# Kernel optimization log

Hardware: AMD Instinct MI355X
Metric: run time of the kernel (lower is better)

## Reference

```python
import jax, jax.numpy as jnp
import numpy as np

B, S, E, HEAD = 8, 2048, 512, 64  # head_size = embeddings_dims // no_of_heads = 512 // 8


def setup_inputs() -> dict:
    key = jax.random.key(0)
    kx, kq, kk, kv, kl = jax.random.split(key, 5)
    x = jax.random.normal(kx, (B, S, E), dtype=jnp.float32)
    # Linear(512 -> 64, bias=False); store as [E, HEAD] so y = x @ W
    Wq = jax.random.normal(kq, (E, HEAD), dtype=jnp.float32) * (E ** -0.5)
    Wk = jax.random.normal(kk, (E, HEAD), dtype=jnp.float32) * (E ** -0.5)
    Wv = jax.random.normal(kv, (E, HEAD), dtype=jnp.float32) * (E ** -0.5)
    # Realistic padding mask: 1 for first `length` tokens, 0 after.
    lengths = jax.random.randint(kl, (B,), S // 2, S + 1)
    mask = (jnp.arange(S)[None, :] < lengths[:, None]).astype(jnp.int32)
    return {"x": x, "Wq": Wq, "Wk": Wk, "Wv": Wv, "mask": mask}


def reference(x, Wq, Wk, Wv, mask):
    # q, k, v: [B, S, HEAD]
    q = x @ Wq
    k = x @ Wk
    v = x @ Wv
    # scores: [B, S, S], scaled by head_size**-0.5 (k.shape[-1] in the original)
    scores = jnp.einsum('bqd,bkd->bqk', q, k) * (HEAD ** -0.5)
    causal = jnp.tril(jnp.ones((S, S), dtype=bool))            # [S, S]
    keep = (mask[:, None, :] != 0) & causal[None, :, :]        # padding mask broadcast over query rows, then causal
    scores = jnp.where(keep, scores, -jnp.inf)
    attn = jax.nn.softmax(scores, axis=-1)                     # [B, S, S]
    out = attn @ v                                             # [B, S, HEAD]
    return out
```

## Files before the change

kernel.cpp:

```cpp
#include <hip/hip_runtime.h>

#define BB 8
#define SS 2048
#define EE 512
#define HD 64
#define CHUNK 256
#define KT 64
#define NCH 8
#define PST 72
#define TST 72
#define XRS 40
#define XKB 1280
#define NITEMS 576

typedef __attribute__((ext_vector_type(8))) short bf16x8;
typedef __attribute__((ext_vector_type(4))) float f32x4;

static __device__ __forceinline__ unsigned short f2bf(float f) {
    unsigned u = __builtin_bit_cast(unsigned, f);
    u = (u + 0x7fffu + ((u >> 16) & 1u)) >> 16;
    return (unsigned short)u;
}
static __device__ __forceinline__ unsigned short f2bf_trunc(float f) {
    return (unsigned short)(__builtin_bit_cast(unsigned, f) >> 16);
}
static __device__ __forceinline__ float bf2f(unsigned short h) {
    unsigned u = ((unsigned)h) << 16;
    return __builtin_bit_cast(float, u);
}

__global__ __launch_bounds__(256) void pack_w_kernel(
    const float* __restrict__ Wq, const float* __restrict__ Wk, const float* __restrict__ Wv,
    unsigned short* __restrict__ Wt) {
    int tid = blockIdx.x * 256 + threadIdx.x;
    if (tid >= 3 * EE * HD) return;
    int w_idx = tid / (EE * HD);
    int rem = tid % (EE * HD);
    int kk = rem / HD, n = rem % HD;
    const float* Wsrc = (w_idx == 0) ? Wq : ((w_idx == 1) ? Wk : Wv);
    float val = Wsrc[kk * HD + n];
    if (w_idx == 0) val *= 0.125f;
    int kb = kk >> 5, kr = kk & 31, quad = kr >> 3, j = kr & 7;
    int t = n >> 4, c = n & 15;
    int lane = quad * 16 + c;
    Wt[w_idx * (EE * HD) + ((kb * 4 + t) * 64 + lane) * 8 + j] = f2bf(val);
}

__global__ __launch_bounds__(256) void qkv_kernel(
    const float* __restrict__ x,
    const unsigned short* __restrict__ Wt,
    unsigned short* __restrict__ q,
    unsigned short* __restrict__ k,
    unsigned short* __restrict__ vT) {
    __shared__ __align__(16) unsigned short Xs[16 * XKB];
    const int tid = threadIdx.x;
    const int lane = tid & 63;
    const int t = tid >> 6;
    const int c = lane & 15, quad = lane >> 4;
    const int r0 = blockIdx.x * 32;

    const float* xt = x + (size_t)r0 * EE;
#pragma unroll
    for (int i = 0; i < 16; ++i) {
        int fi = i * 256 + tid;
        int e4 = fi * 4;
        float4 v4 = *(const float4*)(xt + e4);
        int row = e4 >> 9, col = e4 & 511;
        int kb = col >> 5, cc = col & 31;
        ushort4 pk;
        pk.x = f2bf(v4.x); pk.y = f2bf(v4.y); pk.z = f2bf(v4.z); pk.w = f2bf(v4.w);
        *(ushort4*)(&Xs[kb * XKB + row * XRS + cc]) = pk;
    }
    __syncthreads();

    f32x4 acc[2][3];
#pragma unroll
    for (int rt = 0; rt < 2; ++rt)
        for (int m = 0; m < 3; ++m) acc[rt][m] = (f32x4){0.f, 0.f, 0.f, 0.f};

    const unsigned short* wbase0 = Wt + t * 512 + lane * 8;
#pragma unroll
    for (int kb = 0; kb < EE / 32; ++kb) {
        const unsigned short* wb = wbase0 + kb * 2048;
        bf16x8 bfrag[3];
#pragma unroll
        for (int m = 0; m < 3; ++m) bfrag[m] = *(const bf16x8*)(wb + m * (EE * HD));
#pragma unroll
        for (int rt = 0; rt < 2; ++rt) {
            bf16x8 afrag = *(const bf16x8*)(&Xs[kb * XKB + (rt * 16 + c) * XRS + quad * 8]);
#pragma unroll
            for (int m = 0; m < 3; ++m)
                acc[rt][m] = __builtin_amdgcn_mfma_f32_16x16x32_bf16(afrag, bfrag[m], acc[rt][m], 0, 0, 0);
        }
    }

    const int col = t * 16 + c;
#pragma unroll
    for (int rt = 0; rt < 2; ++rt) {
        const int rb = r0 + rt * 16;
        for (int r = 0; r < 4; ++r) {
            int row = rb + quad * 4 + r;
            q[(size_t)row * HD + col] = f2bf(acc[rt][0][r]);
            k[(size_t)row * HD + col] = f2bf(acc[rt][1][r]);
        }
        int row = rb + quad * 4;
        int b_ = row >> 11, sb = row & (SS - 1);
        ushort4 pk;
        pk.x = f2bf(acc[rt][2][0]); pk.y = f2bf(acc[rt][2][1]);
        pk.z = f2bf(acc[rt][2][2]); pk.w = f2bf(acc[rt][2][3]);
        *(ushort4*)(vT + ((size_t)b_ * HD + col) * SS + sb) = pk;
    }
}

__global__ __launch_bounds__(256, 3) void attn_kernel(
    const unsigned short* __restrict__ q,
    const unsigned short* __restrict__ k,
    const unsigned short* __restrict__ vT,
    const int* __restrict__ mask,
    unsigned short* __restrict__ po,
    float* __restrict__ pl,
    float* __restrict__ out) {
    __shared__ __align__(16) unsigned short Ks[2][64 * TST];
    __shared__ __align__(16) unsigned short Vs[2][64 * TST];
    __shared__ __align__(16) unsigned short Ps[4][16 * PST];
    const int tid = threadIdx.x;
    const int lane = tid & 63, wave = tid >> 6;
    const int c = lane & 15, quad = lane >> 4;

    int t = NITEMS - 1 - blockIdx.x;
    const int b_ = t / 72;
    int r = t % 72;
    int g = 0;
    while ((g + 1) * (g + 2) <= r) ++g;
    int rr = r - g * (g + 1);
    const int Q = 2 * g + rr / (g + 1);
    const int cx = rr % (g + 1);
    const int kstart = cx * CHUNK;
    const int kend = min(kstart + CHUNK, Q * 128 + 128);
    const int ntiles = (kend - kstart) >> 6;
    const int nch_active = Q / 2 + 1;
    const int r0 = Q * 128 + wave * 32;

    const unsigned short* qb_p = q + (size_t)b_ * SS * HD;
    const unsigned short* kb_p = k + (size_t)b_ * SS * HD;
    const unsigned short* vb = vT + (size_t)b_ * HD * SS;
    const int* mb = mask + b_ * SS;

    bf16x8 aq[2][2];
#pragma unroll
    for (int rt = 0; rt < 2; ++rt) {
        const unsigned short* qrow = qb_p + (size_t)(r0 + rt * 16 + c) * HD + quad * 8;
        aq[rt][0] = *(const bf16x8*)(qrow);
        aq[rt][1] = *(const bf16x8*)(qrow + 32);
    }

    f32x4 o[2][4];
    float l_i[2][4];
#pragma unroll
    for (int rt = 0; rt < 2; ++rt)
        for (int tt = 0; tt < 4; ++tt) {
            o[rt][tt] = (f32x4){0.f, 0.f, 0.f, 0.f};
            l_i[rt][tt] = 0.f;
        }

    bf16x8 sk[2], sv[2];
    auto stage_load = [&](int k0) {
        const unsigned short* ksrc = kb_p + (size_t)k0 * HD;
#pragma unroll
        for (int rnd = 0; rnd < 2; ++rnd) {
            int e = (rnd * 256 + tid) * 8;
            sk[rnd] = *(const bf16x8*)(ksrc + e);
            int t8 = rnd * 256 + tid;
            int vr = t8 >> 3, vc = (t8 & 7) * 8;
            sv[rnd] = *(const bf16x8*)(vb + (size_t)vr * SS + k0 + vc);
        }
    };
    auto stage_write = [&](int buf) {
        unsigned short* kd = &Ks[buf][0];
        unsigned short* vd = &Vs[buf][0];
#pragma unroll
        for (int rnd = 0; rnd < 2; ++rnd) {
            int e = (rnd * 256 + tid) * 8;
            int krow = e >> 6, kcol = e & 63;
            *(bf16x8*)(kd + krow * TST + kcol) = sk[rnd];
            int t8 = rnd * 256 + tid;
            int vr = t8 >> 3, vc = (t8 & 7) * 8;
            *(bf16x8*)(vd + vr * TST + vc) = sv[rnd];
        }
    };

    stage_load(kstart);
    stage_write(0);
    for (int kt = 0; kt < ntiles; ++kt) {
        __syncthreads();
        const int k0 = kstart + kt * KT;
        const bool pre = (kt + 1 < ntiles);
        if (pre) stage_load(k0 + KT);
        const unsigned short* ks = &Ks[kt & 1][0];
        const unsigned short* vs = &Vs[kt & 1][0];

        bool mk4[4];
#pragma unroll
        for (int kg = 0; kg < 4; ++kg) mk4[kg] = (mb[k0 + kg * 16 + c] != 0);

        bf16x8 kf[4][2];
#pragma unroll
        for (int kg = 0; kg < 4; ++kg) {
            kf[kg][0] = *(const bf16x8*)(ks + (kg * 16 + c) * TST + quad * 8);
            kf[kg][1] = *(const bf16x8*)(ks + (kg * 16 + c) * TST + 32 + quad * 8);
        }

        bf16x8 pa[2][2];
#pragma unroll
        for (int rt = 0; rt < 2; ++rt) {
            const int rbase = r0 + rt * 16;
            const bool fullc = (k0 + KT <= rbase);
            f32x4 accs4[4];
            __builtin_amdgcn_s_setprio(1);
#pragma unroll
            for (int kg = 0; kg < 4; ++kg) {
                f32x4 a = (f32x4){0.f, 0.f, 0.f, 0.f};
                a = __builtin_amdgcn_mfma_f32_16x16x32_bf16(aq[rt][0], kf[kg][0], a, 0, 0, 0);
                a = __builtin_amdgcn_mfma_f32_16x16x32_bf16(aq[rt][1], kf[kg][1], a, 0, 0, 0);
                accs4[kg] = a;
            }
            __builtin_amdgcn_s_setprio(0);
            unsigned short* pbuf = &Ps[wave][0];
#pragma unroll
            for (int kg = 0; kg < 4; ++kg) {
                int key = k0 + kg * 16 + c;
                bool mk = mk4[kg];
#pragma unroll
                for (int rr2 = 0; rr2 < 4; ++rr2) {
                    int row = rbase + quad * 4 + rr2;
                    bool keep = mk && (fullc || key <= row);
                    float e = __expf(fminf(accs4[kg][rr2], 80.f));
                    float pe = keep ? e : 0.f;
                    l_i[rt][rr2] += pe;
                    pbuf[(quad * 4 + rr2) * PST + kg * 16 + c] = f2bf_trunc(pe);
                }
            }
            pa[rt][0] = *(const bf16x8*)(pbuf + c * PST + quad * 8);
            pa[rt][1] = *(const bf16x8*)(pbuf + c * PST + 32 + quad * 8);
        }

#pragma unroll
        for (int tt = 0; tt < 4; ++tt) {
            bf16x8 bv0 = *(const bf16x8*)(vs + (tt * 16 + c) * TST + quad * 8);
            bf16x8 bv1 = *(const bf16x8*)(vs + (tt * 16 + c) * TST + 32 + quad * 8);
            __builtin_amdgcn_s_setprio(1);
#pragma unroll
            for (int rt = 0; rt < 2; ++rt) {
                o[rt][tt] = __builtin_amdgcn_mfma_f32_16x16x32_bf16(pa[rt][0], bv0, o[rt][tt], 0, 0, 0);
                o[rt][tt] = __builtin_amdgcn_mfma_f32_16x16x32_bf16(pa[rt][1], bv1, o[rt][tt], 0, 0, 0);
            }
            __builtin_amdgcn_s_setprio(0);
        }

        if (pre) stage_write((kt + 1) & 1);
    }

#pragma unroll
    for (int rt = 0; rt < 2; ++rt)
        for (int rr2 = 0; rr2 < 4; ++rr2) {
            float s = l_i[rt][rr2];
            s += __shfl_xor(s, 1);
            s += __shfl_xor(s, 2);
            s += __shfl_xor(s, 4);
            s += __shfl_xor(s, 8);
            l_i[rt][rr2] = s;
        }

    if (nch_active == 1) {
#pragma unroll
        for (int rt = 0; rt < 2; ++rt)
            for (int rr2 = 0; rr2 < 4; ++rr2) {
                int row = r0 + rt * 16 + quad * 4 + rr2;
                float l = l_i[rt][rr2];
                float inv = (l > 0.f) ? 1.f / l : 0.f;
                for (int tt = 0; tt < 4; ++tt)
                    out[((size_t)b_ * SS + row) * HD + tt * 16 + c] = o[rt][tt][rr2] * inv;
            }
        return;
    }

#pragma unroll
    for (int rt = 0; rt < 2; ++rt)
        for (int rr2 = 0; rr2 < 4; ++rr2) {
            int row_abs = r0 + rt * 16 + quad * 4 + rr2;
            int qb_i = row_abs >> 6, rl = row_abs & 63;
            size_t base = (size_t)(b_ * 32 + qb_i) * NCH + cx;
            float l = l_i[rt][rr2];
            float inv = (l > 0.f) ? 1.f / l : 0.f;
            for (int tt = 0; tt < 4; ++tt)
                po[base * 4096 + (size_t)rl * 64 + tt * 16 + c] = f2bf(o[rt][tt][rr2] * inv);
            if (c == 0) pl[base * 64 + rl] = l;
        }
}

__global__ __launch_bounds__(256) void combine_kernel(
    const unsigned short* __restrict__ po,
    const float* __restrict__ pl,
    float* __restrict__ out) {
    int t = blockIdx.x * 256 + threadIdx.x;
    if (t >= BB * (SS - 256) * (HD / 4)) return;
    int d4 = (t & 15) * 4;
    int rg = t >> 4;
    int b_ = rg / (SS - 256);
    int row = 256 + rg % (SS - 256);
    int qb = row >> 6, rl = row & 63;
    int nch = row / CHUNK + 1;
    size_t base = (size_t)(b_ * 32 + qb) * NCH;
    float L = 0.f;
    float acc0 = 0.f, acc1 = 0.f, acc2 = 0.f, acc3 = 0.f;
    for (int cc = 0; cc < nch; ++cc) {
        float l = pl[(base + cc) * 64 + rl];
        L += l;
        ushort4 pk = *(const ushort4*)(po + (base + cc) * 4096 + (size_t)rl * 64 + d4);
        acc0 += l * bf2f(pk.x);
        acc1 += l * bf2f(pk.y);
        acc2 += l * bf2f(pk.z);
        acc3 += l * bf2f(pk.w);
    }
    float inv = (L > 0.f) ? 1.f / L : 0.f;
    float4 o4;
    o4.x = acc0 * inv; o4.y = acc1 * inv; o4.z = acc2 * inv; o4.w = acc3 * inv;
    *(float4*)(out + ((size_t)b_ * SS + row) * HD + d4) = o4;
}

extern "C" void kernel_launch(void* const* d_in, const int* in_sizes, int n_in,
                              void* d_out, int out_size, void* d_ws, size_t ws_size,
                              hipStream_t stream) {
    const float* x = (const float*)d_in[0];
    const float* Wq = (const float*)d_in[1];
    const float* Wk = (const float*)d_in[2];
    const float* Wv = (const float*)d_in[3];
    const int* mask = (const int*)d_in[4];
    float* out = (float*)d_out;

    unsigned short* ws = (unsigned short*)d_ws;
    unsigned short* Wt = ws;
    unsigned short* q = Wt + 3 * EE * HD;
    unsigned short* kk = q + (size_t)BB * SS * HD;
    unsigned short* vT = kk + (size_t)BB * SS * HD;
    unsigned short* po = vT + (size_t)BB * SS * HD;
    float* pl = (float*)(po + (size_t)BB * 32 * NCH * 4096);

    pack_w_kernel<<<dim3((3 * EE * HD + 255) / 256), dim3(256), 0, stream>>>(Wq, Wk, Wv, Wt);
    qkv_kernel<<<dim3(BB * SS / 32), dim3(256), 0, stream>>>(x, Wt, q, kk, vT);
    attn_kernel<<<dim3(NITEMS), dim3(256), 0, stream>>>(q, kk, vT, mask, po, pl, out);
    combine_kernel<<<dim3((BB * (SS - 256) * (HD / 4) + 255) / 256), dim3(256), 0, stream>>>(po, pl, out);
}
```

Baseline: 109.1 us.

## Swap MFMA operand order to produce transposed tiles for vectorized stores

Swaps the A and B operands of the MFMA calls in the QKV projection and in both attention matmuls, so each lane holds four consecutive columns of one row instead of one column across four rows. This allows vectorized ushort4/float4 stores for q, k, output and partials, a packed uint2 write of P into shared memory, int4 mask loads, and a row-sum reduction of two shuffles instead of four per row. The vT store becomes four scalar strided stores, which may cost more in the projection kernel.

```diff
diff --git a/kernel.cpp b/kernel.cpp
--- a/kernel.cpp
+++ b/kernel.cpp
@@ -7,8 +7,8 @@
 #define CHUNK 256
 #define KT 64
 #define NCH 8
-#define PST 72
 #define TST 72
+#define PS32 36
 #define XRS 40
 #define XKB 1280
 #define NITEMS 576
@@ -21,12 +21,14 @@
     u = (u + 0x7fffu + ((u >> 16) & 1u)) >> 16;
     return (unsigned short)u;
 }
-static __device__ __forceinline__ unsigned short f2bf_trunc(float f) {
-    return (unsigned short)(__builtin_bit_cast(unsigned, f) >> 16);
-}
 static __device__ __forceinline__ float bf2f(unsigned short h) {
     unsigned u = ((unsigned)h) << 16;
     return __builtin_bit_cast(float, u);
+}
+static __device__ __forceinline__ unsigned pack2(float lo, float hi) {
+    unsigned ulo = __builtin_bit_cast(unsigned, lo) >> 16;
+    unsigned uhi = __builtin_bit_cast(unsigned, hi) & 0xffff0000u;
+    return uhi | ulo;
 }
 
 __global__ __launch_bounds__(256) void pack_w_kernel(
@@ -82,33 +84,33 @@
 #pragma unroll
     for (int kb = 0; kb < EE / 32; ++kb) {
         const unsigned short* wb = wbase0 + kb * 2048;
-        bf16x8 bfrag[3];
-#pragma unroll
-        for (int m = 0; m < 3; ++m) bfrag[m] = *(const bf16x8*)(wb + m * (EE * HD));
+        bf16x8 wfrag[3];
+#pragma unroll
+        for (int m = 0; m < 3; ++m) wfrag[m] = *(const bf16x8*)(wb + m * (EE * HD));
 #pragma unroll
         for (int rt = 0; rt < 2; ++rt) {
-            bf16x8 afrag = *(const bf16x8*)(&Xs[kb * XKB + (rt * 16 + c) * XRS + quad * 8]);
+            bf16x8 xfrag = *(const bf16x8*)(&Xs[kb * XKB + (rt * 16 + c) * XRS + quad * 8]);
 #pragma unroll
             for (int m = 0; m < 3; ++m)
-                acc[rt][m] = __builtin_amdgcn_mfma_f32_16x16x32_bf16(afrag, bfrag[m], acc[rt][m], 0, 0, 0);
-        }
-    }
-
-    const int col = t * 16 + c;
+                acc[rt][m] = __builtin_amdgcn_mfma_f32_16x16x32_bf16(wfrag[m], xfrag, acc[rt][m], 0, 0, 0);
+        }
+    }
+
+    const int colq = t * 16 + quad * 4;
 #pragma unroll
     for (int rt = 0; rt < 2; ++rt) {
-        const int rb = r0 + rt * 16;
-        for (int r = 0; r < 4; ++r) {
-            int row = rb + quad * 4 + r;
-            q[(size_t)row * HD + col] = f2bf(acc[rt][0][r]);
-            k[(size_t)row * HD + col] = f2bf(acc[rt][1][r]);
-        }
-        int row = rb + quad * 4;
+        const int row = r0 + rt * 16 + c;
+        ushort4 pq, pkk;
+        pq.x = f2bf(acc[rt][0][0]); pq.y = f2bf(acc[rt][0][1]);
+        pq.z = f2bf(acc[rt][0][2]); pq.w = f2bf(acc[rt][0][3]);
+        pkk.x = f2bf(acc[rt][1][0]); pkk.y = f2bf(acc[rt][1][1]);
+        pkk.z = f2bf(acc[rt][1][2]); pkk.w = f2bf(acc[rt][1][3]);
+        *(ushort4*)(q + (size_t)row * HD + colq) = pq;
+        *(ushort4*)(k + (size_t)row * HD + colq) = pkk;
         int b_ = row >> 11, sb = row & (SS - 1);
-        ushort4 pk;
-        pk.x = f2bf(acc[rt][2][0]); pk.y = f2bf(acc[rt][2][1]);
-        pk.z = f2bf(acc[rt][2][2]); pk.w = f2bf(acc[rt][2][3]);
-        *(ushort4*)(vT + ((size_t)b_ * HD + col) * SS + sb) = pk;
+#pragma unroll
+        for (int r = 0; r < 4; ++r)
+            vT[((size_t)b_ * HD + colq + r) * SS + sb] = f2bf(acc[rt][2][r]);
     }
 }
 
@@ -122,7 +124,7 @@
     float* __restrict__ out) {
     __shared__ __align__(16) unsigned short Ks[2][64 * TST];
     __shared__ __align__(16) unsigned short Vs[2][64 * TST];
-    __shared__ __align__(16) unsigned short Ps[4][16 * PST];
+    __shared__ __align__(16) unsigned int Ps32[4][16 * PS32];
     const int tid = threadIdx.x;
     const int lane = tid & 63, wave = tid >> 6;
     const int c = lane & 15, quad = lane >> 4;
@@ -155,13 +157,10 @@
     }
 
     f32x4 o[2][4];
-    float l_i[2][4];
+    float l_part[2] = {0.f, 0.f};
 #pragma unroll
     for (int rt = 0; rt < 2; ++rt)
-        for (int tt = 0; tt < 4; ++tt) {
-            o[rt][tt] = (f32x4){0.f, 0.f, 0.f, 0.f};
-            l_i[rt][tt] = 0.f;
-        }
+        for (int tt = 0; tt < 4; ++tt) o[rt][tt] = (f32x4){0.f, 0.f, 0.f, 0.f};
 
     bf16x8 sk[2], sv[2];
     auto stage_load = [&](int k0) {
@@ -199,9 +198,12 @@
         const unsigned short* ks = &Ks[kt & 1][0];
         const unsigned short* vs = &Vs[kt & 1][0];
 
-        bool mk4[4];
-#pragma unroll
-        for (int kg = 0; kg < 4; ++kg) mk4[kg] = (mb[k0 + kg * 16 + c] != 0);
+        int mks[4][4];
+#pragma unroll
+        for (int kg = 0; kg < 4; ++kg) {
+            int4 mv = *(const int4*)(mb + k0 + kg * 16 + quad * 4);
+            mks[kg][0] = mv.x; mks[kg][1] = mv.y; mks[kg][2] = mv.z; mks[kg][3] = mv.w;
+        }
 
         bf16x8 kf[4][2];
 #pragma unroll
@@ -210,38 +212,43 @@
             kf[kg][1] = *(const bf16x8*)(ks + (kg * 16 + c) * TST + 32 + quad * 8);
         }
 
-        bf16x8 pa[2][2];
+        bf16x8 pB[2][2];
 #pragma unroll
         for (int rt = 0; rt < 2; ++rt) {
             const int rbase = r0 + rt * 16;
+            const int qr = rbase + c;
             const bool fullc = (k0 + KT <= rbase);
             f32x4 accs4[4];
             __builtin_amdgcn_s_setprio(1);
 #pragma unroll
             for (int kg = 0; kg < 4; ++kg) {
                 f32x4 a = (f32x4){0.f, 0.f, 0.f, 0.f};
-                a = __builtin_amdgcn_mfma_f32_16x16x32_bf16(aq[rt][0], kf[kg][0], a, 0, 0, 0);
-                a = __builtin_amdgcn_mfma_f32_16x16x32_bf16(aq[rt][1], kf[kg][1], a, 0, 0, 0);
+                a = __builtin_amdgcn_mfma_f32_16x16x32_bf16(kf[kg][0], aq[rt][0], a, 0, 0, 0);
+                a = __builtin_amdgcn_mfma_f32_16x16x32_bf16(kf[kg][1], aq[rt][1], a, 0, 0, 0);
                 accs4[kg] = a;
             }
             __builtin_amdgcn_s_setprio(0);
-            unsigned short* pbuf = &Ps[wave][0];
+            unsigned int* pb = &Ps32[wave][0];
 #pragma unroll
             for (int kg = 0; kg < 4; ++kg) {
-                int key = k0 + kg * 16 + c;
-                bool mk = mk4[kg];
+                float pe[4];
 #pragma unroll
                 for (int rr2 = 0; rr2 < 4; ++rr2) {
-                    int row = rbase + quad * 4 + rr2;
-                    bool keep = mk && (fullc || key <= row);
+                    int key = k0 + kg * 16 + quad * 4 + rr2;
+                    bool keep = (mks[kg][rr2] != 0) && (fullc || key <= qr);
                     float e = __expf(fminf(accs4[kg][rr2], 80.f));
-                    float pe = keep ? e : 0.f;
-                    l_i[rt][rr2] += pe;
-                    pbuf[(quad * 4 + rr2) * PST + kg * 16 + c] = f2bf_trunc(pe);
+                    float p = keep ? e : 0.f;
+                    l_part[rt] += p;
+                    pe[rr2] = p;
                 }
+                uint2 w2;
+                w2.x = pack2(pe[0], pe[1]);
+                w2.y = pack2(pe[2], pe[3]);
+                *(uint2*)(pb + c * PS32 + kg * 8 + quad * 2) = w2;
             }
-            pa[rt][0] = *(const bf16x8*)(pbuf + c * PST + quad * 8);
-            pa[rt][1] = *(const bf16x8*)(pbuf + c * PST + 32 + quad * 8);
+            const unsigned short* pb16 = (const unsigned short*)pb;
+            pB[rt][0] = *(const bf16x8*)(pb16 + c * (PS32 * 2) + quad * 8);
+            pB[rt][1] = *(const bf16x8*)(pb16 + c * (PS32 * 2) + 32 + quad * 8);
         }
 
 #pragma unroll
@@ -251,8 +258,8 @@
             __builtin_amdgcn_s_setprio(1);
 #pragma unroll
             for (int rt = 0; rt < 2; ++rt) {
-                o[rt][tt] = __builtin_amdgcn_mfma_f32_16x16x32_bf16(pa[rt][0], bv0, o[rt][tt], 0, 0, 0);
-                o[rt][tt] = __builtin_amdgcn_mfma_f32_16x16x32_bf16(pa[rt][1], bv1, o[rt][tt], 0, 0, 0);
+                o[rt][tt] = __builtin_amdgcn_mfma_f32_16x16x32_bf16(bv0, pB[rt][0], o[rt][tt], 0, 0, 0);
+                o[rt][tt] = __builtin_amdgcn_mfma_f32_16x16x32_bf16(bv1, pB[rt][1], o[rt][tt], 0, 0, 0);
             }
             __builtin_amdgcn_s_setprio(0);
         }
@@ -260,42 +267,48 @@
         if (pre) stage_write((kt + 1) & 1);
     }
 
-#pragma unroll
-    for (int rt = 0; rt < 2; ++rt)
-        for (int rr2 = 0; rr2 < 4; ++rr2) {
-            float s = l_i[rt][rr2];
-            s += __shfl_xor(s, 1);
-            s += __shfl_xor(s, 2);
-            s += __shfl_xor(s, 4);
-            s += __shfl_xor(s, 8);
-            l_i[rt][rr2] = s;
-        }
+    float lv[2];
+#pragma unroll
+    for (int rt = 0; rt < 2; ++rt) {
+        float s = l_part[rt];
+        s += __shfl_xor(s, 16);
+        s += __shfl_xor(s, 32);
+        lv[rt] = s;
+    }
 
     if (nch_active == 1) {
 #pragma unroll
-        for (int rt = 0; rt < 2; ++rt)
-            for (int rr2 = 0; rr2 < 4; ++rr2) {
-                int row = r0 + rt * 16 + quad * 4 + rr2;
-                float l = l_i[rt][rr2];
-                float inv = (l > 0.f) ? 1.f / l : 0.f;
-                for (int tt = 0; tt < 4; ++tt)
-                    out[((size_t)b_ * SS + row) * HD + tt * 16 + c] = o[rt][tt][rr2] * inv;
+        for (int rt = 0; rt < 2; ++rt) {
+            int row = r0 + rt * 16 + c;
+            float l = lv[rt];
+            float inv = (l > 0.f) ? 1.f / l : 0.f;
+#pragma unroll
+            for (int tt = 0; tt < 4; ++tt) {
+                float4 o4;
+                o4.x = o[rt][tt][0] * inv; o4.y = o[rt][tt][1] * inv;
+                o4.z = o[rt][tt][2] * inv; o4.w = o[rt][tt][3] * inv;
+                *(float4*)(out + ((size_t)b_ * SS + row) * HD + tt * 16 + quad * 4) = o4;
             }
+        }
         return;
     }
 
 #pragma unroll
-    for (int rt = 0; rt < 2; ++rt)
-        for (int rr2 = 0; rr2 < 4; ++rr2) {
-            int row_abs = r0 + rt * 16 + quad * 4 + rr2;
-            int qb_i = row_abs >> 6, rl = row_abs & 63;
-            size_t base = (size_t)(b_ * 32 + qb_i) * NCH + cx;
-            float l = l_i[rt][rr2];
-            float inv = (l > 0.f) ? 1.f / l : 0.f;
-            for (int tt = 0; tt < 4; ++tt)
-                po[base * 4096 + (size_t)rl * 64 + tt * 16 + c] = f2bf(o[rt][tt][rr2] * inv);
-            if (c == 0) pl[base * 64 + rl] = l;
-        }
+    for (int rt = 0; rt < 2; ++rt) {
+        int row_abs = r0 + rt * 16 + c;
+        int qb_i = row_abs >> 6, rl = row_abs & 63;
+        size_t base = (size_t)(b_ * 32 + qb_i) * NCH + cx;
+        float l = lv[rt];
+        float inv = (l > 0.f) ? 1.f / l : 0.f;
+#pragma unroll
+        for (int tt = 0; tt < 4; ++tt) {
+            ushort4 pk;
+            pk.x = f2bf(o[rt][tt][0] * inv); pk.y = f2bf(o[rt][tt][1] * inv);
+            pk.z = f2bf(o[rt][tt][2] * inv); pk.w = f2bf(o[rt][tt][3] * inv);
+            *(ushort4*)(po + base * 4096 + (size_t)rl * 64 + tt * 16 + quad * 4) = pk;
+        }
+        if (quad == 0) pl[base * 64 + rl] = l;
+    }
 }
 
 __global__ __launch_bounds__(256) void combine_kernel(
```

Result: no change. 109.9 us (+0.7%).
